# Kernel tuning notes

Hardware: AMD Instinct MI355X
Metric: run time of the kernel (lower is better)

Reference implementation:

```python
import jax, jax.numpy as jnp
import numpy as np

NEG_INF = -jnp.inf


def setup_inputs() -> dict:
    key = jax.random.key(0)
    ks = jax.random.split(key, 6)
    B, S, D, DK = 8, 2048, 1024, 128
    x = jax.random.normal(ks[0], (B, S, D), dtype=jnp.float32)
    context = jax.random.normal(ks[1], (B, S, D), dtype=jnp.float32)
    # torch nn.Linear weights: [out_features, in_features]
    Wq = jax.random.normal(ks[2], (DK, D), dtype=jnp.float32) * 0.02
    Wk = jax.random.normal(ks[3], (DK, D), dtype=jnp.float32) * 0.02
    Wv = jax.random.normal(ks[4], (DK, D), dtype=jnp.float32) * 0.02
    # valid lengths in [S//2, S] so every row has at least one valid key
    batch_lengths = jax.random.randint(ks[5], (B,), S // 2, S + 1, dtype=jnp.int32)
    return {
        "x": x,
        "context": context,
        "Wq": Wq,
        "Wk": Wk,
        "Wv": Wv,
        "batch_lengths": batch_lengths,
        "max_len": S,
        "decoding": 1,
    }


def reference(x, context, Wq, Wk, Wv, batch_lengths, max_len, decoding):
    B, S, D = x.shape
    dk = Wq.shape[0]
    pos = jnp.arange(S)
    # outputMask: 1.0 for t < length, else 0.0; broadcast over feature dim dk
    valid = pos[None, :] < batch_lengths[:, None]            # [B, S]
    mask = valid[:, :, None].astype(x.dtype)                 # [B, S, 1] (broadcast to dk)
    Q = jnp.einsum('bsd,kd->bsk', context, Wq) * mask        # [B, S, dk]
    K = jnp.einsum('bsd,kd->bsk', context, Wk) * mask
    V = jnp.einsum('bsd,kd->bsk', x, Wv) * mask
    energy = jnp.einsum('bqk,bjk->bqj', Q, K)                # [B, S, S]
    # attnMask: -inf at padded key positions (j >= length)
    key_pad = ~valid                                         # [B, S]
    energy = jnp.where(key_pad[:, None, :], NEG_INF, energy)
    if decoding:
        # causal: energy[:, i, j] = -inf for j > i (the python double loop)
        causal = pos[:, None] < pos[None, :]                 # [S, S], True above diag
        energy = jnp.where(causal[None, :, :], NEG_INF, energy)
    score = jax.nn.softmax(energy / jnp.sqrt(jnp.asarray(dk, x.dtype)), axis=-1)
    return jnp.einsum('bqj,bjk->bqk', score, V)              # [B, S, dk]
```

## Files before the change

kernel.cpp:

```cpp
#include <hip/hip_runtime.h>
#include <hip/hip_bf16.h>

#define BB 8
#define SS 2048
#define DD 1024
#define DKK 128

using bf16x8  = __attribute__((ext_vector_type(8))) __bf16;
using floatx4 = __attribute__((ext_vector_type(4))) float;
using intx4   = __attribute__((ext_vector_type(4))) int;

__device__ __forceinline__ void lds16(const void* g, void* l) {
    __builtin_amdgcn_global_load_lds((const __attribute__((address_space(1))) void*)g,
                                     (__attribute__((address_space(3))) void*)l, 16, 0, 0);
}

__device__ __forceinline__ int pack2(float a, float b) {
    union { __bf16 h; unsigned short u; } ua, ub;
    ua.h = (__bf16)a; ub.h = (__bf16)b;
    return (int)(ua.u | ((unsigned)ub.u << 16));
}

__global__ __launch_bounds__(256) void convw_kernel(
    const float* __restrict__ Wq, const float* __restrict__ Wk,
    const float* __restrict__ Wv, __bf16* __restrict__ Wt)
{
    const int z = blockIdx.y;
    const float* W = (z == 0) ? Wq : (z == 1) ? Wk : Wv;
    const int t  = blockIdx.x * 256 + threadIdx.x;
    const int n  = t >> 7;
    const int k0 = (t & 127) * 8;
    float4 f0 = *(const float4*)(W + n * DD + k0);
    float4 f1 = *(const float4*)(W + n * DD + k0 + 4);
    bf16x8 v;
    v[0]=(__bf16)f0.x; v[1]=(__bf16)f0.y; v[2]=(__bf16)f0.z; v[3]=(__bf16)f0.w;
    v[4]=(__bf16)f1.x; v[5]=(__bf16)f1.y; v[6]=(__bf16)f1.z; v[7]=(__bf16)f1.w;
    const int kb  = (k0 >> 3) & 7;
    const int kbs = kb ^ (n & 7);
    *(bf16x8*)(Wt + (size_t)z * 131072 + ((k0 >> 6) * 128 + n) * 64 + kbs * 8) = v;
}

__global__ __launch_bounds__(256) void proj_kernel(
    const float* __restrict__ x, const float* __restrict__ ctx,
    const __bf16* __restrict__ Wt, const int* __restrict__ lengths,
    __bf16* __restrict__ Qb, __bf16* __restrict__ Kb, __bf16* __restrict__ Vt)
{
    __shared__ __align__(16) __bf16 SH[20992];
    __bf16* Abuf = SH;
    __bf16* Wl0  = SH + 4608;
    __bf16* Wl1  = SH + 12800;
    __bf16* T    = SH + 4608;

    const int isV = blockIdx.x >= 256;
    const int m0  = (isV ? blockIdx.x - 256 : blockIdx.x) * 64;
    const int b   = m0 >> 11;
    const int s0  = m0 & (SS - 1);
    const int len = lengths[b];
    if (s0 >= len) return;

    const int tid  = threadIdx.x;
    const int wave = tid >> 6;
    const int lane = tid & 63;
    const int quad = lane >> 4;
    const int l16  = lane & 15;
    const int wm   = wave >> 1;
    const int wn   = wave & 1;

    const float*  A  = isV ? x : ctx;
    const __bf16* W0 = isV ? (Wt + 262144) : Wt;
    const __bf16* W1 = Wt + 131072;

    const int r    = tid >> 2;
    const int kseg = (tid & 3) * 16;
    const float* Ab = A + (size_t)(m0 + r) * DD + kseg;
    const int  wel  = tid * 8;

    floatx4 acc[2][2][4];
#pragma unroll
    for (int m_ = 0; m_ < 2; ++m_)
#pragma unroll
        for (int i = 0; i < 2; ++i)
#pragma unroll
            for (int j = 0; j < 4; ++j) acc[m_][i][j] = (floatx4){0.f,0.f,0.f,0.f};

    float4 pf[4];
    bf16x8 wr0[4], wr1[4];
#pragma unroll
    for (int i = 0; i < 4; ++i) pf[i] = *(const float4*)(Ab + i * 4);
#pragma unroll
    for (int i = 0; i < 4; ++i)
        wr0[i] = *(const bf16x8*)(W0 + i * 2048 + wel);
    if (!isV)
#pragma unroll
        for (int i = 0; i < 4; ++i)
            wr1[i] = *(const bf16x8*)(W1 + i * 2048 + wel);

    for (int t = 0; t < 16; ++t) {
        __syncthreads();
        {
            bf16x8 c0, c1;
            c0[0]=(__bf16)pf[0].x; c0[1]=(__bf16)pf[0].y; c0[2]=(__bf16)pf[0].z; c0[3]=(__bf16)pf[0].w;
            c0[4]=(__bf16)pf[1].x; c0[5]=(__bf16)pf[1].y; c0[6]=(__bf16)pf[1].z; c0[7]=(__bf16)pf[1].w;
            c1[0]=(__bf16)pf[2].x; c1[1]=(__bf16)pf[2].y; c1[2]=(__bf16)pf[2].z; c1[3]=(__bf16)pf[2].w;
            c1[4]=(__bf16)pf[3].x; c1[5]=(__bf16)pf[3].y; c1[6]=(__bf16)pf[3].z; c1[7]=(__bf16)pf[3].w;
            *(bf16x8*)&Abuf[r * 72 + kseg]     = c0;
            *(bf16x8*)&Abuf[r * 72 + kseg + 8] = c1;
        }
#pragma unroll
        for (int i = 0; i < 4; ++i) *(bf16x8*)&Wl0[i * 2048 + wel] = wr0[i];
        if (!isV)
#pragma unroll
            for (int i = 0; i < 4; ++i) *(bf16x8*)&Wl1[i * 2048 + wel] = wr1[i];

        if (t < 15) {
            const float* ap = Ab + (t + 1) * 64;
#pragma unroll
            for (int i = 0; i < 4; ++i) pf[i] = *(const float4*)(ap + i * 4);
            const __bf16* wp0 = W0 + (size_t)(t + 1) * 8192 + wel;
#pragma unroll
            for (int i = 0; i < 4; ++i) wr0[i] = *(const bf16x8*)(wp0 + i * 2048);
            if (!isV) {
                const __bf16* wp1 = W1 + (size_t)(t + 1) * 8192 + wel;
#pragma unroll
                for (int i = 0; i < 4; ++i) wr1[i] = *(const bf16x8*)(wp1 + i * 2048);
            }
        }
        __syncthreads();

#pragma unroll
        for (int kh = 0; kh < 2; ++kh) {
            bf16x8 af[2];
#pragma unroll
            for (int mt = 0; mt < 2; ++mt)
                af[mt] = *(const bf16x8*)&Abuf[(wm*32 + mt*16 + l16) * 72 + kh*32 + quad*8];
            const int kb = kh * 4 + quad;
#pragma unroll
            for (int nt = 0; nt < 4; ++nt) {
                const int n = wn * 64 + nt * 16 + l16;
                const int off = n * 64 + ((kb ^ (n & 7)) << 3);
                bf16x8 w0 = *(const bf16x8*)&Wl0[off];
#pragma unroll
                for (int mt = 0; mt < 2; ++mt)
                    acc[0][mt][nt] = __builtin_amdgcn_mfma_f32_16x16x32_bf16(af[mt], w0, acc[0][mt][nt], 0, 0, 0);
                if (!isV) {
                    bf16x8 w1 = *(const bf16x8*)&Wl1[off];
#pragma unroll
                    for (int mt = 0; mt < 2; ++mt)
                        acc[1][mt][nt] = __builtin_amdgcn_mfma_f32_16x16x32_bf16(af[mt], w1, acc[1][mt][nt], 0, 0, 0);
                }
            }
        }
    }

    if (!isV) {
#pragma unroll
        for (int mt = 0; mt < 2; ++mt)
#pragma unroll
            for (int rr = 0; rr < 4; ++rr) {
                const int row = m0 + wm*32 + mt*16 + quad*4 + rr;
                const float mk = ((row & (SS - 1)) < len) ? 1.f : 0.f;
#pragma unroll
                for (int nt = 0; nt < 4; ++nt) {
                    const int col = wn*64 + nt*16 + l16;
                    Qb[(size_t)row * DKK + col] = (__bf16)(acc[0][mt][nt][rr] * mk);
                    Kb[(size_t)row * DKK + col] = (__bf16)(acc[1][mt][nt][rr] * mk);
                }
            }
    } else {
        __syncthreads();
#pragma unroll
        for (int mt = 0; mt < 2; ++mt)
#pragma unroll
            for (int nt = 0; nt < 4; ++nt)
#pragma unroll
                for (int rr = 0; rr < 4; ++rr) {
                    const int s = wm*32 + mt*16 + quad*4 + rr;
                    const int n = wn*64 + nt*16 + l16;
                    const float mk = (s0 + s < len) ? 1.f : 0.f;
                    T[n * 72 + s] = (__bf16)(acc[0][mt][nt][rr] * mk);
                }
        __syncthreads();
        const int n = tid >> 1, h = tid & 1;
        __bf16* dst = Vt + (size_t)b * DKK * SS + (size_t)n * SS + s0 + h * 32;
#pragma unroll
        for (int i = 0; i < 4; ++i)
            *(bf16x8*)(dst + i * 8) = *(const bf16x8*)&T[n * 72 + h * 32 + i * 8];
    }
}

__global__ __launch_bounds__(256) void vmean_kernel(
    const __bf16* __restrict__ Vt, const int* __restrict__ lengths,
    float* __restrict__ Vmean)
{
    const int b   = blockIdx.x >> 3;
    const int g3  = blockIdx.x & 7;
    const int len = lengths[b];
    const int tid = threadIdx.x;
    const int n   = g3 * 16 + (tid >> 4);
    const int sl  = (tid & 15) * 128;
    const __bf16* src = Vt + (size_t)b * DKK * SS + (size_t)n * SS + sl;
    float s = 0.f;
#pragma unroll
    for (int i = 0; i < 16; ++i) {
        bf16x8 v = *(const bf16x8*)(src + i * 8);
#pragma unroll
        for (int j = 0; j < 8; ++j)
            s += (sl + i * 8 + j < len) ? (float)v[j] : 0.f;
    }
#pragma unroll
    for (int off = 1; off < 16; off <<= 1)
        s += __shfl_xor(s, off, 64);
    if ((tid & 15) == 0) Vmean[b * DKK + n] = s / (float)len;
}

__global__ __launch_bounds__(256) void attn_kernel(
    const __bf16* __restrict__ Qb, const __bf16* __restrict__ Kb,
    const __bf16* __restrict__ Vt, const int* __restrict__ lengths,
    const float* __restrict__ Vmean, float* __restrict__ out)
{
    __shared__ __align__(16) __bf16 KB[2 * 8192];

    const int b    = blockIdx.x & 7;
    const int ii   = blockIdx.x >> 3;
    const int qt   = (ii < 32) ? (63 - ii) : (ii - 32);
    const int qw   = qt * 32;
    const int len  = lengths[b];
    const int tid  = threadIdx.x;
    const int wave = tid >> 6;
    const int lane = tid & 63;
    const int quad = lane >> 4;
    const int l16  = lane & 15;
    const int sub  = wave >> 1;
    const int half = wave & 1;

    if (qw >= len) {
        const int c8 = (tid & 15) * 8;
        const float4 v0 = *(const float4*)(Vmean + b * DKK + c8);
        const float4 v1 = *(const float4*)(Vmean + b * DKK + c8 + 4);
#pragma unroll
        for (int pass = 0; pass < 2; ++pass) {
            const int row = pass * 16 + (tid >> 4);
            float* op = out + (size_t)(b * SS + qw + row) * DKK + c8;
            *(float4*)op = v0; *(float4*)(op + 4) = v1;
        }
        return;
    }

    const int jmax = min(qw + 32, len);
    const int nc   = (jmax + 63) >> 6;
    const __bf16* Kbase = Kb + (size_t)b * SS * DKK;
    const __bf16* Vbase = Vt + (size_t)b * DKK * SS;

    bf16x8 qfrag[4];
    {
        const __bf16* Qbase = Qb + (size_t)(b * SS + qw + sub * 16) * DKK;
#pragma unroll
        for (int cc = 0; cc < 4; ++cc)
            qfrag[cc] = *(const bf16x8*)(Qbase + (size_t)l16 * DKK + cc * 32 + quad * 8);
    }

    floatx4 oacc[8];
#pragma unroll
    for (int nt = 0; nt < 8; ++nt) oacc[nt] = (floatx4){0.f,0.f,0.f,0.f};
    float lsum = 0.f;
    const float scale = 0.08838834764831845f;
    const int   iq    = qw + sub * 16 + l16;
    const int   sw7   = l16 & 7;

    auto stageK = [&](int buf, int j0) {
#pragma unroll
        for (int i = 0; i < 4; ++i) {
            const int c   = wave * 4 + i;
            const int row = c * 4 + quad;
            const int sb  = l16 ^ (row & 7);
            lds16(Kbase + (size_t)(j0 + row) * DKK + sb * 8,
                  KB + buf * 8192 + c * 512);
        }
    };

    auto process = [&](int buf, int j0) {
        const int kbas = buf * 8192;
        bf16x8 vf[8];
#pragma unroll
        for (int nt = 0; nt < 8; ++nt)
            vf[nt] = *(const bf16x8*)(
                Vbase + (size_t)(nt*16 + l16) * SS + j0 + half*32 + quad*8);

        floatx4 st[2];
#pragma unroll
        for (int jt = 0; jt < 2; ++jt) {
            st[jt] = (floatx4){0.f,0.f,0.f,0.f};
#pragma unroll
            for (int cc = 0; cc < 4; ++cc) {
                bf16x8 kf = *(const bf16x8*)(
                    KB + kbas + ((half*2 + jt)*16 + l16) * 128 + (((cc*4 + quad) ^ sw7) * 8));
                st[jt] = __builtin_amdgcn_mfma_f32_16x16x32_bf16(
                    kf, qfrag[cc], st[jt], 0, 0, 0);
            }
        }
        int pk[2][2];
#pragma unroll
        for (int jt = 0; jt < 2; ++jt) {
            float p[4];
#pragma unroll
            for (int rr = 0; rr < 4; ++rr) {
                const int j = j0 + half*32 + jt*16 + quad*4 + rr;
                p[rr] = (j > iq || j >= len) ? 0.f : __expf(st[jt][rr] * scale - 8.f);
                lsum += p[rr];
            }
            pk[jt][0] = pack2(p[0], p[1]);
            pk[jt][1] = pack2(p[2], p[3]);
        }
        const int a0 = (((quad & 1) << 5) + l16) << 2;
        const int a1 = a0 + 64;
        const int r00 = __builtin_amdgcn_ds_bpermute(a0, pk[0][0]);
        const int r01 = __builtin_amdgcn_ds_bpermute(a0, pk[0][1]);
        const int r02 = __builtin_amdgcn_ds_bpermute(a0, pk[1][0]);
        const int r03 = __builtin_amdgcn_ds_bpermute(a0, pk[1][1]);
        const int r10 = __builtin_amdgcn_ds_bpermute(a1, pk[0][0]);
        const int r11 = __builtin_amdgcn_ds_bpermute(a1, pk[0][1]);
        const int r12 = __builtin_amdgcn_ds_bpermute(a1, pk[1][0]);
        const int r13 = __builtin_amdgcn_ds_bpermute(a1, pk[1][1]);
        const bool hi = quad >= 2;
        union { intx4 i; bf16x8 h; } u;
        u.i = (intx4){ hi ? r02 : r00, hi ? r03 : r01,
                       hi ? r12 : r10, hi ? r13 : r11 };
#pragma unroll
        for (int nt = 0; nt < 8; ++nt)
            oacc[nt] = __builtin_amdgcn_mfma_f32_16x16x32_bf16(
                u.h, vf[nt], oacc[nt], 0, 0, 0);
    };

    stageK(0, 0);
    __syncthreads();
    for (int c = 0; c < nc; ++c) {
        const int cur = c & 1;
        if (c + 1 < nc) stageK(cur ^ 1, (c + 1) * 64);
        process(cur, c * 64);
        __syncthreads();
    }

    lsum += __shfl_xor(lsum, 16, 64);
    lsum += __shfl_xor(lsum, 32, 64);

    float* Ored = (float*)KB;
    float* Lred = (float*)KB + 4096;
    if (half) {
#pragma unroll
        for (int nt = 0; nt < 8; ++nt)
#pragma unroll
            for (int rr = 0; rr < 4; ++rr)
                Ored[sub*2048 + (quad*4 + rr)*128 + nt*16 + l16] = oacc[nt][rr];
        if (lane < 16) Lred[sub*16 + l16] = lsum;
    }
    __syncthreads();
    if (!half) {
        const float lt = lsum + Lred[sub*16 + l16];
        float inv[4];
#pragma unroll
        for (int rr = 0; rr < 4; ++rr)
            inv[rr] = 1.f / __shfl(lt, quad * 4 + rr, 64);
#pragma unroll
        for (int nt = 0; nt < 8; ++nt)
#pragma unroll
            for (int rr = 0; rr < 4; ++rr)
                out[(size_t)(b * SS + qw + sub*16 + quad*4 + rr) * DKK + nt*16 + l16] =
                    (oacc[nt][rr] + Ored[sub*2048 + (quad*4 + rr)*128 + nt*16 + l16]) * inv[rr];
    }
}

extern "C" void kernel_launch(void* const* d_in, const int* in_sizes, int n_in,
                              void* d_out, int out_size, void* d_ws, size_t ws_size,
                              hipStream_t stream) {
    const float* x   = (const float*)d_in[0];
    const float* ctx = (const float*)d_in[1];
    const float* Wq  = (const float*)d_in[2];
    const float* Wk  = (const float*)d_in[3];
    const float* Wv  = (const float*)d_in[4];
    const int* lengths = (const int*)d_in[5];
    float* out = (float*)d_out;

    char* ws = (char*)d_ws;
    __bf16* Wt = (__bf16*)ws;
    __bf16* Qb = (__bf16*)(ws + 786432);
    __bf16* Kb = (__bf16*)(ws + 786432 + 4194304);
    __bf16* Vt = (__bf16*)(ws + 786432 + 8388608);
    float*  Vm = (float*) (ws + 786432 + 12582912);

    convw_kernel<<<dim3(64, 3), 256, 0, stream>>>(Wq, Wk, Wv, Wt);
    proj_kernel<<<512, 256, 0, stream>>>(x, ctx, Wt, lengths, Qb, Kb, Vt);
    vmean_kernel<<<64, 256, 0, stream>>>(Vt, lengths, Vm);
    attn_kernel<<<512, 256, 0, stream>>>(Qb, Kb, Vt, lengths, Vm, out);
}
```

Measured before the change: 210.8 us.

## Split attention into 16-row query tiles with four waves splitting keys

Each attention block now handles 16 query rows instead of 32. All four waves share the same Q tile and split each 128-key chunk four ways, so the grid doubles to 1024 blocks, tiles are ordered longest first, and the final reduction merges partial outputs and row sums from three waves. The aim is finer load balance across the causal triangle and less wasted work on the diagonal. In exchange, K and V are reloaded for every block, doubling their global traffic, LDS use per block doubles, and the cross-wave reduction gets larger.

```diff
diff --git a/kernel.cpp b/kernel.cpp
--- a/kernel.cpp
+++ b/kernel.cpp
@@ -218,42 +218,36 @@
     const __bf16* __restrict__ Vt, const int* __restrict__ lengths,
     const float* __restrict__ Vmean, float* __restrict__ out)
 {
-    __shared__ __align__(16) __bf16 KB[2 * 8192];
+    __shared__ __align__(16) __bf16 KB[2 * 16384];
 
     const int b    = blockIdx.x & 7;
-    const int ii   = blockIdx.x >> 3;
-    const int qt   = (ii < 32) ? (63 - ii) : (ii - 32);
-    const int qw   = qt * 32;
+    const int t    = 127 - (blockIdx.x >> 3);
+    const int qw   = t * 16;
     const int len  = lengths[b];
     const int tid  = threadIdx.x;
     const int wave = tid >> 6;
     const int lane = tid & 63;
     const int quad = lane >> 4;
     const int l16  = lane & 15;
-    const int sub  = wave >> 1;
-    const int half = wave & 1;
 
     if (qw >= len) {
-        const int c8 = (tid & 15) * 8;
+        const int row = tid >> 4;
+        const int c8  = (tid & 15) * 8;
         const float4 v0 = *(const float4*)(Vmean + b * DKK + c8);
         const float4 v1 = *(const float4*)(Vmean + b * DKK + c8 + 4);
-#pragma unroll
-        for (int pass = 0; pass < 2; ++pass) {
-            const int row = pass * 16 + (tid >> 4);
-            float* op = out + (size_t)(b * SS + qw + row) * DKK + c8;
-            *(float4*)op = v0; *(float4*)(op + 4) = v1;
-        }
+        float* op = out + (size_t)(b * SS + qw + row) * DKK + c8;
+        *(float4*)op = v0; *(float4*)(op + 4) = v1;
         return;
     }
 
-    const int jmax = min(qw + 32, len);
-    const int nc   = (jmax + 63) >> 6;
+    const int jmax = min(qw + 16, len);
+    const int nc   = (jmax + 127) >> 7;
     const __bf16* Kbase = Kb + (size_t)b * SS * DKK;
     const __bf16* Vbase = Vt + (size_t)b * DKK * SS;
 
     bf16x8 qfrag[4];
     {
-        const __bf16* Qbase = Qb + (size_t)(b * SS + qw + sub * 16) * DKK;
+        const __bf16* Qbase = Qb + (size_t)(b * SS + qw) * DKK;
 #pragma unroll
         for (int cc = 0; cc < 4; ++cc)
             qfrag[cc] = *(const bf16x8*)(Qbase + (size_t)l16 * DKK + cc * 32 + quad * 8);
@@ -264,27 +258,31 @@
     for (int nt = 0; nt < 8; ++nt) oacc[nt] = (floatx4){0.f,0.f,0.f,0.f};
     float lsum = 0.f;
     const float scale = 0.08838834764831845f;
-    const int   iq    = qw + sub * 16 + l16;
+    const int   iq    = qw + l16;
     const int   sw7   = l16 & 7;
+    const int   h32   = wave * 32;
 
     auto stageK = [&](int buf, int j0) {
 #pragma unroll
-        for (int i = 0; i < 4; ++i) {
-            const int c   = wave * 4 + i;
+        for (int i = 0; i < 8; ++i) {
+            const int c   = wave * 8 + i;
             const int row = c * 4 + quad;
             const int sb  = l16 ^ (row & 7);
             lds16(Kbase + (size_t)(j0 + row) * DKK + sb * 8,
-                  KB + buf * 8192 + c * 512);
+                  KB + buf * 16384 + c * 512);
         }
     };
 
     auto process = [&](int buf, int j0) {
-        const int kbas = buf * 8192;
+        const int kbas = buf * 16384;
         bf16x8 vf[8];
-#pragma unroll
-        for (int nt = 0; nt < 8; ++nt)
-            vf[nt] = *(const bf16x8*)(
-                Vbase + (size_t)(nt*16 + l16) * SS + j0 + half*32 + quad*8);
+        {
+            int jv = j0 + h32 + quad * 8;
+            if (jv >= len) jv = 0;
+#pragma unroll
+            for (int nt = 0; nt < 8; ++nt)
+                vf[nt] = *(const bf16x8*)(Vbase + (size_t)(nt*16 + l16) * SS + jv);
+        }
 
         floatx4 st[2];
 #pragma unroll
@@ -293,7 +291,7 @@
 #pragma unroll
             for (int cc = 0; cc < 4; ++cc) {
                 bf16x8 kf = *(const bf16x8*)(
-                    KB + kbas + ((half*2 + jt)*16 + l16) * 128 + (((cc*4 + quad) ^ sw7) * 8));
+                    KB + kbas + (h32 + jt*16 + l16) * 128 + (((cc*4 + quad) ^ sw7) * 8));
                 st[jt] = __builtin_amdgcn_mfma_f32_16x16x32_bf16(
                     kf, qfrag[cc], st[jt], 0, 0, 0);
             }
@@ -304,7 +302,7 @@
             float p[4];
 #pragma unroll
             for (int rr = 0; rr < 4; ++rr) {
-                const int j = j0 + half*32 + jt*16 + quad*4 + rr;
+                const int j = j0 + h32 + jt*16 + quad*4 + rr;
                 p[rr] = (j > iq || j >= len) ? 0.f : __expf(st[jt][rr] * scale - 8.f);
                 lsum += p[rr];
             }
@@ -335,8 +333,8 @@
     __syncthreads();
     for (int c = 0; c < nc; ++c) {
         const int cur = c & 1;
-        if (c + 1 < nc) stageK(cur ^ 1, (c + 1) * 64);
-        process(cur, c * 64);
+        if (c + 1 < nc) stageK(cur ^ 1, (c + 1) * 128);
+        process(cur, c * 128);
         __syncthreads();
     }
 
@@ -344,18 +342,18 @@
     lsum += __shfl_xor(lsum, 32, 64);
 
     float* Ored = (float*)KB;
-    float* Lred = (float*)KB + 4096;
-    if (half) {
+    float* Lred = (float*)KB + 3 * 2048;
+    if (wave != 0) {
 #pragma unroll
         for (int nt = 0; nt < 8; ++nt)
 #pragma unroll
             for (int rr = 0; rr < 4; ++rr)
-                Ored[sub*2048 + (quad*4 + rr)*128 + nt*16 + l16] = oacc[nt][rr];
-        if (lane < 16) Lred[sub*16 + l16] = lsum;
+                Ored[(wave-1)*2048 + (quad*4 + rr)*128 + nt*16 + l16] = oacc[nt][rr];
+        if (lane < 16) Lred[(wave-1)*16 + l16] = lsum;
     }
     __syncthreads();
-    if (!half) {
-        const float lt = lsum + Lred[sub*16 + l16];
+    if (wave == 0) {
+        const float lt = lsum + Lred[l16] + Lred[16 + l16] + Lred[32 + l16];
         float inv[4];
 #pragma unroll
         for (int rr = 0; rr < 4; ++rr)
@@ -363,9 +361,11 @@
 #pragma unroll
         for (int nt = 0; nt < 8; ++nt)
 #pragma unroll
-            for (int rr = 0; rr < 4; ++rr)
-                out[(size_t)(b * SS + qw + sub*16 + quad*4 + rr) * DKK + nt*16 + l16] =
-                    (oacc[nt][rr] + Ored[sub*2048 + (quad*4 + rr)*128 + nt*16 + l16]) * inv[rr];
+            for (int rr = 0; rr < 4; ++rr) {
+                const int idx = (quad*4 + rr)*128 + nt*16 + l16;
+                out[(size_t)(b * SS + qw + quad*4 + rr) * DKK + nt*16 + l16] =
+                    (oacc[nt][rr] + Ored[idx] + Ored[2048 + idx] + Ored[4096 + idx]) * inv[rr];
+            }
     }
 }
 
@@ -390,5 +390,5 @@
     convw_kernel<<<dim3(64, 3), 256, 0, stream>>>(Wq, Wk, Wv, Wt);
     proj_kernel<<<512, 256, 0, stream>>>(x, ctx, Wt, lengths, Qb, Kb, Vt);
     vmean_kernel<<<64, 256, 0, stream>>>(Vt, lengths, Vm);
-    attn_kernel<<<512, 256, 0, stream>>>(Qb, Kb, Vt, lengths, Vm, out);
-}
+    attn_kernel<<<1024, 256, 0, stream>>>(Qb, Kb, Vt, lengths, Vm, out);
+}
```

Result: no change. 208.1 us (-1.3%).
